# Kernel tuning notes

Measured on AMD Instinct MI355X. Metric: run time of the kernel, lower is better.

## Reference

```python
import jax, jax.numpy as jnp
import numpy as np

N = 100000   # nodes
DEG = 16     # in-degree per node
E = N * DEG  # edges
D = 64       # embedding_dim


def mobius_addition(x, y, c):
    xy = jnp.sum(x * y, axis=-1, keepdims=True)
    x2 = jnp.sum(x * x, axis=-1, keepdims=True)
    y2 = jnp.sum(y * y, axis=-1, keepdims=True)
    num = (1 + 2 * c * xy + c * y2) * x + (1 - c * x2) * y
    den = 1 + 2 * c * xy + c * c * x2 * y2
    return num / den


def exp_map(x, v, c):
    vn = jnp.linalg.norm(v, axis=-1, keepdims=True)
    sc = jnp.sqrt(c)
    second = jnp.tanh(sc * vn / 2) * v / (sc * vn)
    return mobius_addition(x, second, c)


def log_map(x, y, c):
    add = mobius_addition(-x, y, c)
    an = jnp.linalg.norm(add, axis=-1, keepdims=True)
    sc = jnp.sqrt(c)
    return 2 / sc * jnp.arctanh(sc * an) * add / an


def setup_inputs() -> dict:
    key = jax.random.key(0)
    ks = jax.random.split(key, 6)
    # scale so points are well inside the Poincare ball (atanh domain)
    x = jax.random.normal(ks[0], (N, D), jnp.float32) * 0.01
    src = jax.random.randint(ks[1], (E,), 0, N, dtype=jnp.int32)
    # every node gets exactly DEG in-edges -> no isolated nodes (avoids 0/0 in exp_map)
    dst = jnp.repeat(jnp.arange(N, dtype=jnp.int32), DEG)
    s = 1.0 / np.sqrt(D)
    Wq = jax.random.normal(ks[2], (D, D), jnp.float32) * s
    Wk = jax.random.normal(ks[3], (D, D), jnp.float32) * s
    Wv = jax.random.normal(ks[4], (D, D), jnp.float32) * s
    bq = jnp.zeros((D,), jnp.float32)
    bk = jnp.zeros((D,), jnp.float32)
    bv = jnp.zeros((D,), jnp.float32)
    curvature = jnp.ones((1,), jnp.float32)
    return {"x": x, "curvature": curvature, "Wq": Wq, "bq": bq, "Wk": Wk,
            "bk": bk, "Wv": Wv, "bv": bv, "src": src, "dst": dst}


def reference(x, curvature, Wq, bq, Wk, bk, Wv, bv, src, dst):
    c = curvature  # (1,), broadcasts against (N,1) keepdim norms
    n = x.shape[0]
    origin = jnp.zeros_like(x[:1])  # (1, D)
    tangent = log_map(origin, x, c)  # (N, D)
    # torch nn.Linear: y = x @ W.T + b
    q = tangent @ Wq.T + bq
    k = tangent @ Wk.T + bk
    v = tangent @ Wv.T + bv
    scale = jnp.asarray(x.shape[-1] ** 0.5, x.dtype)
    # per-edge score: <k[src], q[dst]> / sqrt(d)
    scores = jnp.einsum('ed,ed->e', k[src], q[dst]) / scale  # (E,)
    # segment (per-dst) softmax over incoming edges
    smax = jax.ops.segment_max(scores, dst, num_segments=n)
    ex = jnp.exp(scores - smax[dst])
    ssum = jax.ops.segment_sum(ex, dst, num_segments=n)
    alpha = ex / ssum[dst]  # (E,)
    # weighted scatter-sum of src values
    h = jax.ops.segment_sum(alpha[:, None] * v[src], dst, num_segments=n)  # (N, D)
    return exp_map(origin, h, c)
```

## Files before the change

kernel.cpp:

```cpp
#include <hip/hip_runtime.h>
#include <hip/hip_bf16.h>
#include <math.h>


typedef __attribute__((ext_vector_type(8))) short bf16x8;
typedef __attribute__((ext_vector_type(4))) float f32x4;
typedef __attribute__((ext_vector_type(2))) float f32x2;

static __device__ __forceinline__ short f2bf(float f) {
    union { __hip_bfloat16 h; short s; } u; u.h = __float2bfloat16(f); return u.s;
}

#define UBCVT(F, SRC, IDX) asm("v_cvt_f32_ubyte" IDX " %0, %1" : "=v"(F) : "v"(SRC))

#define TSTRIDE 72
#define SQF     68
#define SKSTR   72
#define SVSTR   68

__global__ __launch_bounds__(256) void qkv_kernel(
    const float* __restrict__ x,
    const float* __restrict__ cur,
    const float* __restrict__ Wq, const float* __restrict__ bq,
    const float* __restrict__ Wk, const float* __restrict__ bk,
    const float* __restrict__ Wv, const float* __restrict__ bv,
    float* __restrict__ qf, unsigned char* __restrict__ kvl,
    float* __restrict__ vs, int N)
{
    __shared__ short tL[128 * TSTRIDE];
    __shared__ float sqf[16 * SQF];
    __shared__ unsigned char sk[16 * SKSTR];
    __shared__ float svf[16 * SVSTR];
    const int tid = threadIdx.x;
    const int w = tid >> 6, lane = tid & 63;
    const int blockBase = blockIdx.x * 128;
    const float sc = __builtin_amdgcn_sqrtf(cur[0]);

    const int rr = lane >> 2, p = lane & 3;
    #pragma unroll
    for (int it = 0; it < 2; ++it) {
        const int rloc = w * 32 + it * 16 + rr;
        int row = blockBase + rloc; if (row >= N) row = N - 1;
        const float4* xr = (const float4*)(x + (size_t)row * 64 + p * 16);
        float4 x0 = xr[0], x1 = xr[1], x2 = xr[2], x3 = xr[3];
        float pn = x0.x*x0.x + x0.y*x0.y + x0.z*x0.z + x0.w*x0.w
                 + x1.x*x1.x + x1.y*x1.y + x1.z*x1.z + x1.w*x1.w
                 + x2.x*x2.x + x2.y*x2.y + x2.z*x2.z + x2.w*x2.w
                 + x3.x*x3.x + x3.y*x3.y + x3.z*x3.z + x3.w*x3.w;
        pn += __shfl_xor(pn, 1, 64);
        pn += __shfl_xor(pn, 2, 64);
        float z = sc * __builtin_amdgcn_sqrtf(pn);
        float ts = (z > 1e-12f)
            ? (__logf((1.0f + z) * __builtin_amdgcn_rcpf(1.0f - z))
               * __builtin_amdgcn_rcpf(z))
            : 2.0f;
        bf16x8 t0, t1;
        t0[0]=f2bf(ts*x0.x); t0[1]=f2bf(ts*x0.y); t0[2]=f2bf(ts*x0.z); t0[3]=f2bf(ts*x0.w);
        t0[4]=f2bf(ts*x1.x); t0[5]=f2bf(ts*x1.y); t0[6]=f2bf(ts*x1.z); t0[7]=f2bf(ts*x1.w);
        t1[0]=f2bf(ts*x2.x); t1[1]=f2bf(ts*x2.y); t1[2]=f2bf(ts*x2.z); t1[3]=f2bf(ts*x2.w);
        t1[4]=f2bf(ts*x3.x); t1[5]=f2bf(ts*x3.y); t1[6]=f2bf(ts*x3.z); t1[7]=f2bf(ts*x3.w);
        bf16x8* dst = (bf16x8*)&tL[rloc * TSTRIDE + p * 16];
        dst[0] = t0; dst[1] = t1;
    }
    __syncthreads();

    const int n16 = lane & 15, quad = lane >> 4;
    bf16x8 Bf[3][2];
    float bias[3];
    int matv[3], col0v[3];
    #pragma unroll
    for (int tt = 0; tt < 3; ++tt) {
        const int tile = w * 3 + tt;
        const int mat = tile >> 2;
        const int col0 = (tile & 3) * 16;
        matv[tt] = mat; col0v[tt] = col0;
        const float* Wm = (mat == 0) ? Wq : (mat == 1) ? Wk : Wv;
        const float* bm = (mat == 0) ? bq : (mat == 1) ? bk : bv;
        const float* srcp = Wm + (col0 + n16) * 64 + quad * 8;
        #pragma unroll
        for (int h = 0; h < 2; ++h) {
            float4 a = *(const float4*)(srcp + h * 32);
            float4 b = *(const float4*)(srcp + h * 32 + 4);
            bf16x8 f;
            f[0]=f2bf(a.x); f[1]=f2bf(a.y); f[2]=f2bf(a.z); f[3]=f2bf(a.w);
            f[4]=f2bf(b.x); f[5]=f2bf(b.y); f[6]=f2bf(b.z); f[7]=f2bf(b.w);
            Bf[tt][h] = f;
        }
        bias[tt] = bm[col0 + n16];
    }

    const int crow = tid >> 4;
    const int c8   = tid & 15;

    for (int nt = 0; nt < 8; ++nt) {
        const short* ar = &tL[(nt * 16 + n16) * TSTRIDE + quad * 8];
        bf16x8 A0 = *(const bf16x8*)ar;
        bf16x8 A1 = *(const bf16x8*)(ar + 32);
        #pragma unroll
        for (int tt = 0; tt < 3; ++tt) {
            f32x4 acc = { bias[tt], bias[tt], bias[tt], bias[tt] };
            acc = __builtin_amdgcn_mfma_f32_16x16x32_bf16(A0, Bf[tt][0], acc, 0, 0, 0);
            acc = __builtin_amdgcn_mfma_f32_16x16x32_bf16(A1, Bf[tt][1], acc, 0, 0, 0);
            const int mat = matv[tt], col0 = col0v[tt];
            #pragma unroll
            for (int r4 = 0; r4 < 4; ++r4) {
                const int rl = quad * 4 + r4;
                const int c  = col0 + n16;
                if (mat == 0) {
                    sqf[rl * SQF + c] = acc[r4];
                } else if (mat == 1) {
                    int pk = __builtin_amdgcn_cvt_pk_fp8_f32(acc[r4], acc[r4], 0, false);
                    sk[rl * SKSTR + c] = (unsigned char)(pk & 0xff);
                } else {
                    svf[rl * SVSTR + c] = acc[r4];
                }
            }
        }
        __syncthreads();

        const int node = blockBase + nt * 16 + crow;
        {
            f32x4 v4 = *(const f32x4*)&svf[crow * SVSTR + c8 * 4];
            float m = fmaxf(fmaxf(fabsf(v4[0]), fabsf(v4[1])),
                            fmaxf(fabsf(v4[2]), fabsf(v4[3])));
            m = fmaxf(m, __shfl_xor(m, 1, 64));
            m = fmaxf(m, __shfl_xor(m, 2, 64));
            m = fmaxf(m, __shfl_xor(m, 4, 64));
            m = fmaxf(m, __shfl_xor(m, 8, 64));
            float rm = fmaxf(m, 1e-20f);
            float inv = 127.0f * __builtin_amdgcn_rcpf(rm);
            float scale = rm * (1.0f / 127.0f);
            int i0 = __float2int_rn(v4[0] * inv) + 128;
            int i1 = __float2int_rn(v4[1] * inv) + 128;
            int i2 = __float2int_rn(v4[2] * inv) + 128;
            int i3 = __float2int_rn(v4[3] * inv) + 128;
            unsigned pk = (unsigned)(i0 & 255) | ((unsigned)(i1 & 255) << 8)
                        | ((unsigned)(i2 & 255) << 16) | ((unsigned)(i3 & 255) << 24);
            if (node < N) {
                *(f32x4*)(qf + (size_t)node * 64 + c8 * 4) =
                    *(const f32x4*)&sqf[crow * SQF + c8 * 4];
                *(unsigned*)(kvl + (size_t)node * 128 + c8 * 4) =
                    *(const unsigned*)&sk[crow * SKSTR + c8 * 4];
                *(unsigned*)(kvl + (size_t)node * 128 + 64 + c8 * 4) = pk;
                if (c8 == 0) vs[node] = scale;
            }
        }
        __syncthreads();
    }
}

__global__ __launch_bounds__(256) void attn_kernel(
    const float* __restrict__ qf, const unsigned char* __restrict__ kvl,
    const float* __restrict__ vs, const int* __restrict__ src,
    const float* __restrict__ cur,
    float* __restrict__ out, int N)
{
    __shared__ float aA[4][2][16];
    const int tid = threadIdx.x;
    const int w = tid >> 6, lane = tid & 63;
    int n0 = blockIdx.x * 8 + w;
    int n1 = n0 + 4;
    if (n0 >= N) n0 = N - 1;
    if (n1 >= N) n1 = N - 1;

    const int j = lane >> 2, p = lane & 3;
    const int g = lane >> 4, m = lane & 15;
    const float c0 = cur[0];

    const int* srow0 = src + n0 * 16;
    const int* srow1 = src + n1 * 16;
    const int  sj0 = srow0[j];
    const int4 s40 = *(const int4*)(srow0 + (g << 2));
    const int  sj1 = srow1[j];
    const int4 s41 = *(const int4*)(srow1 + (g << 2));

    const unsigned dimoff = (unsigned)(m << 2);
    const unsigned v00 = ((unsigned)s40.x << 7) + dimoff;
    const unsigned v01 = ((unsigned)s40.y << 7) + dimoff;
    const unsigned v02 = ((unsigned)s40.z << 7) + dimoff;
    const unsigned v03 = ((unsigned)s40.w << 7) + dimoff;
    const unsigned vr00 = *(const unsigned*)(kvl + 64 + v00);
    const unsigned vr01 = *(const unsigned*)(kvl + 64 + v01);
    const unsigned vr02 = *(const unsigned*)(kvl + 64 + v02);
    const unsigned vr03 = *(const unsigned*)(kvl + 64 + v03);
    const unsigned v10 = ((unsigned)s41.x << 7) + dimoff;
    const unsigned v11 = ((unsigned)s41.y << 7) + dimoff;
    const unsigned v12 = ((unsigned)s41.z << 7) + dimoff;
    const unsigned v13 = ((unsigned)s41.w << 7) + dimoff;
    const unsigned vr10 = *(const unsigned*)(kvl + 64 + v10);
    const unsigned vr11 = *(const unsigned*)(kvl + 64 + v11);
    const unsigned vr12 = *(const unsigned*)(kvl + 64 + v12);
    const unsigned vr13 = *(const unsigned*)(kvl + 64 + v13);

    const unsigned ko0 = ((unsigned)sj0 << 7) + (unsigned)(p << 4);
    const unsigned ko1 = ((unsigned)sj1 << 7) + (unsigned)(p << 4);
    const uint4 kd0 = *(const uint4*)(kvl + ko0);
    const uint4 kd1 = *(const uint4*)(kvl + ko1);
    const float sjs0 = vs[sj0];
    const float sjs1 = vs[sj1];

    const float* qp0 = qf + (size_t)n0 * 64 + (p << 4);
    const float4 q00 = *(const float4*)(qp0);
    const float4 q01 = *(const float4*)(qp0 + 4);
    const float4 q02 = *(const float4*)(qp0 + 8);
    const float4 q03 = *(const float4*)(qp0 + 12);

    float acc0 = 0.f;
    {
        f32x2 k0 = __builtin_amdgcn_cvt_pk_f32_fp8(kd0.x, false);
        f32x2 k1 = __builtin_amdgcn_cvt_pk_f32_fp8(kd0.x, true);
        acc0 = fmaf(k0[0], q00.x, acc0); acc0 = fmaf(k0[1], q00.y, acc0);
        acc0 = fmaf(k1[0], q00.z, acc0); acc0 = fmaf(k1[1], q00.w, acc0);
        k0 = __builtin_amdgcn_cvt_pk_f32_fp8(kd0.y, false);
        k1 = __builtin_amdgcn_cvt_pk_f32_fp8(kd0.y, true);
        acc0 = fmaf(k0[0], q01.x, acc0); acc0 = fmaf(k0[1], q01.y, acc0);
        acc0 = fmaf(k1[0], q01.z, acc0); acc0 = fmaf(k1[1], q01.w, acc0);
        k0 = __builtin_amdgcn_cvt_pk_f32_fp8(kd0.z, false);
        k1 = __builtin_amdgcn_cvt_pk_f32_fp8(kd0.z, true);
        acc0 = fmaf(k0[0], q02.x, acc0); acc0 = fmaf(k0[1], q02.y, acc0);
        acc0 = fmaf(k1[0], q02.z, acc0); acc0 = fmaf(k1[1], q02.w, acc0);
        k0 = __builtin_amdgcn_cvt_pk_f32_fp8(kd0.w, false);
        k1 = __builtin_amdgcn_cvt_pk_f32_fp8(kd0.w, true);
        acc0 = fmaf(k0[0], q03.x, acc0); acc0 = fmaf(k0[1], q03.y, acc0);
        acc0 = fmaf(k1[0], q03.z, acc0); acc0 = fmaf(k1[1], q03.w, acc0);
    }

    const float* qp1 = qf + (size_t)n1 * 64 + (p << 4);
    const float4 q10 = *(const float4*)(qp1);
    const float4 q11 = *(const float4*)(qp1 + 4);
    const float4 q12 = *(const float4*)(qp1 + 8);
    const float4 q13 = *(const float4*)(qp1 + 12);

    acc0 += __shfl_xor(acc0, 1, 64);
    acc0 += __shfl_xor(acc0, 2, 64);
    float ex0 = __builtin_amdgcn_exp2f(acc0 * (0.125f * 1.44269504f));
    float ss0 = ex0;
    #pragma unroll
    for (int mm = 4; mm < 64; mm <<= 1) ss0 += __shfl_xor(ss0, mm, 64);
    float as0 = ex0 * sjs0 * __builtin_amdgcn_rcpf(ss0);
    if (p == 0) aA[w][0][j] = as0;

    float acc1 = 0.f;
    {
        f32x2 k0 = __builtin_amdgcn_cvt_pk_f32_fp8(kd1.x, false);
        f32x2 k1 = __builtin_amdgcn_cvt_pk_f32_fp8(kd1.x, true);
        acc1 = fmaf(k0[0], q10.x, acc1); acc1 = fmaf(k0[1], q10.y, acc1);
        acc1 = fmaf(k1[0], q10.z, acc1); acc1 = fmaf(k1[1], q10.w, acc1);
        k0 = __builtin_amdgcn_cvt_pk_f32_fp8(kd1.y, false);
        k1 = __builtin_amdgcn_cvt_pk_f32_fp8(kd1.y, true);
        acc1 = fmaf(k0[0], q11.x, acc1); acc1 = fmaf(k0[1], q11.y, acc1);
        acc1 = fmaf(k1[0], q11.z, acc1); acc1 = fmaf(k1[1], q11.w, acc1);
        k0 = __builtin_amdgcn_cvt_pk_f32_fp8(kd1.z, false);
        k1 = __builtin_amdgcn_cvt_pk_f32_fp8(kd1.z, true);
        acc1 = fmaf(k0[0], q12.x, acc1); acc1 = fmaf(k0[1], q12.y, acc1);
        acc1 = fmaf(k1[0], q12.z, acc1); acc1 = fmaf(k1[1], q12.w, acc1);
        k0 = __builtin_amdgcn_cvt_pk_f32_fp8(kd1.w, false);
        k1 = __builtin_amdgcn_cvt_pk_f32_fp8(kd1.w, true);
        acc1 = fmaf(k0[0], q13.x, acc1); acc1 = fmaf(k0[1], q13.y, acc1);
        acc1 = fmaf(k1[0], q13.z, acc1); acc1 = fmaf(k1[1], q13.w, acc1);
    }

    acc1 += __shfl_xor(acc1, 1, 64);
    acc1 += __shfl_xor(acc1, 2, 64);
    float ex1 = __builtin_amdgcn_exp2f(acc1 * (0.125f * 1.44269504f));
    float ss1 = ex1;
    #pragma unroll
    for (int mm = 4; mm < 64; mm <<= 1) ss1 += __shfl_xor(ss1, mm, 64);
    float as1 = ex1 * sjs1 * __builtin_amdgcn_rcpf(ss1);
    if (p == 0) aA[w][1][j] = as1;

    __builtin_amdgcn_wave_barrier();
    const float4 a40 = *(const float4*)&aA[w][0][g << 2];
    const float4 a41 = *(const float4*)&aA[w][1][g << 2];
    const float sa0 = (a40.x + a40.y) + (a40.z + a40.w);
    const float sa1 = (a41.x + a41.y) + (a41.z + a41.w);

    float h00 = 0.f, h01 = 0.f, h02 = 0.f, h03 = 0.f;
    float h10 = 0.f, h11 = 0.f, h12 = 0.f, h13 = 0.f;
    {
        float f0, f1, f2, f3;
        UBCVT(f0, vr00, "0"); UBCVT(f1, vr00, "1"); UBCVT(f2, vr00, "2"); UBCVT(f3, vr00, "3");
        h00 = fmaf(a40.x, f0, h00); h01 = fmaf(a40.x, f1, h01);
        h02 = fmaf(a40.x, f2, h02); h03 = fmaf(a40.x, f3, h03);
        UBCVT(f0, vr01, "0"); UBCVT(f1, vr01, "1"); UBCVT(f2, vr01, "2"); UBCVT(f3, vr01, "3");
        h00 = fmaf(a40.y, f0, h00); h01 = fmaf(a40.y, f1, h01);
        h02 = fmaf(a40.y, f2, h02); h03 = fmaf(a40.y, f3, h03);
        UBCVT(f0, vr02, "0"); UBCVT(f1, vr02, "1"); UBCVT(f2, vr02, "2"); UBCVT(f3, vr02, "3");
        h00 = fmaf(a40.z, f0, h00); h01 = fmaf(a40.z, f1, h01);
        h02 = fmaf(a40.z, f2, h02); h03 = fmaf(a40.z, f3, h03);
        UBCVT(f0, vr03, "0"); UBCVT(f1, vr03, "1"); UBCVT(f2, vr03, "2"); UBCVT(f3, vr03, "3");
        h00 = fmaf(a40.w, f0, h00); h01 = fmaf(a40.w, f1, h01);
        h02 = fmaf(a40.w, f2, h02); h03 = fmaf(a40.w, f3, h03);

        UBCVT(f0, vr10, "0"); UBCVT(f1, vr10, "1"); UBCVT(f2, vr10, "2"); UBCVT(f3, vr10, "3");
        h10 = fmaf(a41.x, f0, h10); h11 = fmaf(a41.x, f1, h11);
        h12 = fmaf(a41.x, f2, h12); h13 = fmaf(a41.x, f3, h13);
        UBCVT(f0, vr11, "0"); UBCVT(f1, vr11, "1"); UBCVT(f2, vr11, "2"); UBCVT(f3, vr11, "3");
        h10 = fmaf(a41.y, f0, h10); h11 = fmaf(a41.y, f1, h11);
        h12 = fmaf(a41.y, f2, h12); h13 = fmaf(a41.y, f3, h13);
        UBCVT(f0, vr12, "0"); UBCVT(f1, vr12, "1"); UBCVT(f2, vr12, "2"); UBCVT(f3, vr12, "3");
        h10 = fmaf(a41.z, f0, h10); h11 = fmaf(a41.z, f1, h11);
        h12 = fmaf(a41.z, f2, h12); h13 = fmaf(a41.z, f3, h13);
        UBCVT(f0, vr13, "0"); UBCVT(f1, vr13, "1"); UBCVT(f2, vr13, "2"); UBCVT(f3, vr13, "3");
        h10 = fmaf(a41.w, f0, h10); h11 = fmaf(a41.w, f1, h11);
        h12 = fmaf(a41.w, f2, h12); h13 = fmaf(a41.w, f3, h13);
    }
    const float cr0 = 128.0f * sa0;
    const float cr1 = 128.0f * sa1;
    h00 -= cr0; h01 -= cr0; h02 -= cr0; h03 -= cr0;
    h10 -= cr1; h11 -= cr1; h12 -= cr1; h13 -= cr1;

    h00 += __shfl_xor(h00, 16, 64); h01 += __shfl_xor(h01, 16, 64);
    h02 += __shfl_xor(h02, 16, 64); h03 += __shfl_xor(h03, 16, 64);
    h10 += __shfl_xor(h10, 16, 64); h11 += __shfl_xor(h11, 16, 64);
    h12 += __shfl_xor(h12, 16, 64); h13 += __shfl_xor(h13, 16, 64);
    h00 += __shfl_xor(h00, 32, 64); h01 += __shfl_xor(h01, 32, 64);
    h02 += __shfl_xor(h02, 32, 64); h03 += __shfl_xor(h03, 32, 64);
    h10 += __shfl_xor(h10, 32, 64); h11 += __shfl_xor(h11, 32, 64);
    h12 += __shfl_xor(h12, 32, 64); h13 += __shfl_xor(h13, 32, 64);

    float n20 = h00*h00 + h01*h01 + h02*h02 + h03*h03;
    float n21 = h10*h10 + h11*h11 + h12*h12 + h13*h13;
    n20 += __shfl_xor(n20, 1, 64); n21 += __shfl_xor(n21, 1, 64);
    n20 += __shfl_xor(n20, 2, 64); n21 += __shfl_xor(n21, 2, 64);
    n20 += __shfl_xor(n20, 4, 64); n21 += __shfl_xor(n21, 4, 64);
    n20 += __shfl_xor(n20, 8, 64); n21 += __shfl_xor(n21, 8, 64);
    const float sc = __builtin_amdgcn_sqrtf(c0);
    float z0 = sc * __builtin_amdgcn_sqrtf(n20);
    float z1 = sc * __builtin_amdgcn_sqrtf(n21);
    float e0 = __builtin_amdgcn_exp2f(z0 * 1.44269504f);
    float e1 = __builtin_amdgcn_exp2f(z1 * 1.44269504f);
    float sc0 = (z0 > 1e-12f)
        ? ((e0 - 1.0f) * __builtin_amdgcn_rcpf(z0 * (e0 + 1.0f))) : 0.5f;
    float sc1 = (z1 > 1e-12f)
        ? ((e1 - 1.0f) * __builtin_amdgcn_rcpf(z1 * (e1 + 1.0f))) : 0.5f;
    if (lane < 16) {
        float4 o0 = make_float4(sc0 * h00, sc0 * h01, sc0 * h02, sc0 * h03);
        float4 o1 = make_float4(sc1 * h10, sc1 * h11, sc1 * h12, sc1 * h13);
        *(float4*)(out + (size_t)n0 * 64 + (lane << 2)) = o0;
        *(float4*)(out + (size_t)n1 * 64 + (lane << 2)) = o1;
    }
}

extern "C" void kernel_launch(void* const* d_in, const int* in_sizes, int n_in,
                              void* d_out, int out_size, void* d_ws, size_t ws_size,
                              hipStream_t stream)
{
    const float* x   = (const float*)d_in[0];
    const float* cur = (const float*)d_in[1];
    const float* Wq  = (const float*)d_in[2];
    const float* bq  = (const float*)d_in[3];
    const float* Wk  = (const float*)d_in[4];
    const float* bk  = (const float*)d_in[5];
    const float* Wv  = (const float*)d_in[6];
    const float* bv  = (const float*)d_in[7];
    const int* src = (const int*)d_in[8];

    const int N = in_sizes[0] / 64;

    float*          qf  = (float*)d_ws;
    unsigned char*  kvl = (unsigned char*)(qf + (size_t)N * 64);
    float*          vsc = (float*)(kvl + (size_t)N * 128);

    const int blocks1 = (N + 127) / 128;
    const int blocks2 = (N + 7) / 8;
    qkv_kernel<<<blocks1, 256, 0, stream>>>(x, cur, Wq, bq, Wk, bk, Wv, bv,
                                            qf, kvl, vsc, N);
    attn_kernel<<<blocks2, 256, 0, stream>>>(qf, kvl, vsc, src, cur,
                                             (float*)d_out, N);
}
```

Measured before the change: 156.0 us.

## Store Q in bf16 and make attention kernel persistent with src prefetch

Q is now written by the projection kernel as bf16 instead of fp32, which halves Q write and read traffic, and the attention kernel widens it back to float with shifts. The attention kernel becomes a grid-stride persistent loop over a capped grid of 2048 blocks, with each wave handling two adjacent nodes and prefetching the next iteration's src indices. This cuts launch and tail overhead and overlaps index loads with compute, but it adds bf16 rounding error on Q and a loop-carried dependency that may limit latency hiding.

Measured after the change: 154.5 us. Within noise of the previous version (-0.9%).

```diff
diff --git a/kernel.cpp b/kernel.cpp
--- a/kernel.cpp
+++ b/kernel.cpp
@@ -10,11 +10,17 @@
 static __device__ __forceinline__ short f2bf(float f) {
     union { __hip_bfloat16 h; short s; } u; u.h = __float2bfloat16(f); return u.s;
 }
+static __device__ __forceinline__ float bflo(unsigned u) {
+    return __uint_as_float(u << 16);
+}
+static __device__ __forceinline__ float bfhi(unsigned u) {
+    return __uint_as_float(u & 0xffff0000u);
+}
 
 #define UBCVT(F, SRC, IDX) asm("v_cvt_f32_ubyte" IDX " %0, %1" : "=v"(F) : "v"(SRC))
 
 #define TSTRIDE 72
-#define SQF     68
+#define SQSTR   72
 #define SKSTR   72
 #define SVSTR   68
 
@@ -24,11 +30,11 @@
     const float* __restrict__ Wq, const float* __restrict__ bq,
     const float* __restrict__ Wk, const float* __restrict__ bk,
     const float* __restrict__ Wv, const float* __restrict__ bv,
-    float* __restrict__ qf, unsigned char* __restrict__ kvl,
+    unsigned short* __restrict__ qb, unsigned char* __restrict__ kvl,
     float* __restrict__ vs, int N)
 {
     __shared__ short tL[128 * TSTRIDE];
-    __shared__ float sqf[16 * SQF];
+    __shared__ short sq[16 * SQSTR];
     __shared__ unsigned char sk[16 * SKSTR];
     __shared__ float svf[16 * SVSTR];
     const int tid = threadIdx.x;
@@ -107,7 +113,7 @@
                 const int rl = quad * 4 + r4;
                 const int c  = col0 + n16;
                 if (mat == 0) {
-                    sqf[rl * SQF + c] = acc[r4];
+                    sq[rl * SQSTR + c] = f2bf(acc[r4]);
                 } else if (mat == 1) {
                     int pk = __builtin_amdgcn_cvt_pk_fp8_f32(acc[r4], acc[r4], 0, false);
                     sk[rl * SKSTR + c] = (unsigned char)(pk & 0xff);
@@ -137,8 +143,8 @@
             unsigned pk = (unsigned)(i0 & 255) | ((unsigned)(i1 & 255) << 8)
                         | ((unsigned)(i2 & 255) << 16) | ((unsigned)(i3 & 255) << 24);
             if (node < N) {
-                *(f32x4*)(qf + (size_t)node * 64 + c8 * 4) =
-                    *(const f32x4*)&sqf[crow * SQF + c8 * 4];
+                *(uint2*)(qb + (size_t)node * 64 + c8 * 4) =
+                    *(const uint2*)&sq[crow * SQSTR + c8 * 4];
                 *(unsigned*)(kvl + (size_t)node * 128 + c8 * 4) =
                     *(const unsigned*)&sk[crow * SKSTR + c8 * 4];
                 *(unsigned*)(kvl + (size_t)node * 128 + 64 + c8 * 4) = pk;
@@ -150,7 +156,7 @@
 }
 
 __global__ __launch_bounds__(256) void attn_kernel(
-    const float* __restrict__ qf, const unsigned char* __restrict__ kvl,
+    const unsigned short* __restrict__ qb, const unsigned char* __restrict__ kvl,
     const float* __restrict__ vs, const int* __restrict__ src,
     const float* __restrict__ cur,
     float* __restrict__ out, int N)
@@ -158,187 +164,198 @@
     __shared__ float aA[4][2][16];
     const int tid = threadIdx.x;
     const int w = tid >> 6, lane = tid & 63;
-    int n0 = blockIdx.x * 8 + w;
-    int n1 = n0 + 4;
-    if (n0 >= N) n0 = N - 1;
-    if (n1 >= N) n1 = N - 1;
+    const int wg = blockIdx.x * 4 + w;
+    const int stride = gridDim.x * 8;
 
     const int j = lane >> 2, p = lane & 3;
     const int g = lane >> 4, m = lane & 15;
     const float c0 = cur[0];
-
-    const int* srow0 = src + n0 * 16;
-    const int* srow1 = src + n1 * 16;
-    const int  sj0 = srow0[j];
-    const int4 s40 = *(const int4*)(srow0 + (g << 2));
-    const int  sj1 = srow1[j];
-    const int4 s41 = *(const int4*)(srow1 + (g << 2));
-
+    const float sc = __builtin_amdgcn_sqrtf(c0);
     const unsigned dimoff = (unsigned)(m << 2);
-    const unsigned v00 = ((unsigned)s40.x << 7) + dimoff;
-    const unsigned v01 = ((unsigned)s40.y << 7) + dimoff;
-    const unsigned v02 = ((unsigned)s40.z << 7) + dimoff;
-    const unsigned v03 = ((unsigned)s40.w << 7) + dimoff;
-    const unsigned vr00 = *(const unsigned*)(kvl + 64 + v00);
-    const unsigned vr01 = *(const unsigned*)(kvl + 64 + v01);
-    const unsigned vr02 = *(const unsigned*)(kvl + 64 + v02);
-    const unsigned vr03 = *(const unsigned*)(kvl + 64 + v03);
-    const unsigned v10 = ((unsigned)s41.x << 7) + dimoff;
-    const unsigned v11 = ((unsigned)s41.y << 7) + dimoff;
-    const unsigned v12 = ((unsigned)s41.z << 7) + dimoff;
-    const unsigned v13 = ((unsigned)s41.w << 7) + dimoff;
-    const unsigned vr10 = *(const unsigned*)(kvl + 64 + v10);
-    const unsigned vr11 = *(const unsigned*)(kvl + 64 + v11);
-    const unsigned vr12 = *(const unsigned*)(kvl + 64 + v12);
-    const unsigned vr13 = *(const unsigned*)(kvl + 64 + v13);
-
-    const unsigned ko0 = ((unsigned)sj0 << 7) + (unsigned)(p << 4);
-    const unsigned ko1 = ((unsigned)sj1 << 7) + (unsigned)(p << 4);
-    const uint4 kd0 = *(const uint4*)(kvl + ko0);
-    const uint4 kd1 = *(const uint4*)(kvl + ko1);
-    const float sjs0 = vs[sj0];
-    const float sjs1 = vs[sj1];
-
-    const float* qp0 = qf + (size_t)n0 * 64 + (p << 4);
-    const float4 q00 = *(const float4*)(qp0);
-    const float4 q01 = *(const float4*)(qp0 + 4);
-    const float4 q02 = *(const float4*)(qp0 + 8);
-    const float4 q03 = *(const float4*)(qp0 + 12);
-
-    float acc0 = 0.f;
-    {
-        f32x2 k0 = __builtin_amdgcn_cvt_pk_f32_fp8(kd0.x, false);
-        f32x2 k1 = __builtin_amdgcn_cvt_pk_f32_fp8(kd0.x, true);
-        acc0 = fmaf(k0[0], q00.x, acc0); acc0 = fmaf(k0[1], q00.y, acc0);
-        acc0 = fmaf(k1[0], q00.z, acc0); acc0 = fmaf(k1[1], q00.w, acc0);
-        k0 = __builtin_amdgcn_cvt_pk_f32_fp8(kd0.y, false);
-        k1 = __builtin_amdgcn_cvt_pk_f32_fp8(kd0.y, true);
-        acc0 = fmaf(k0[0], q01.x, acc0); acc0 = fmaf(k0[1], q01.y, acc0);
-        acc0 = fmaf(k1[0], q01.z, acc0); acc0 = fmaf(k1[1], q01.w, acc0);
-        k0 = __builtin_amdgcn_cvt_pk_f32_fp8(kd0.z, false);
-        k1 = __builtin_amdgcn_cvt_pk_f32_fp8(kd0.z, true);
-        acc0 = fmaf(k0[0], q02.x, acc0); acc0 = fmaf(k0[1], q02.y, acc0);
-        acc0 = fmaf(k1[0], q02.z, acc0); acc0 = fmaf(k1[1], q02.w, acc0);
-        k0 = __builtin_amdgcn_cvt_pk_f32_fp8(kd0.w, false);
-        k1 = __builtin_amdgcn_cvt_pk_f32_fp8(kd0.w, true);
-        acc0 = fmaf(k0[0], q03.x, acc0); acc0 = fmaf(k0[1], q03.y, acc0);
-        acc0 = fmaf(k1[0], q03.z, acc0); acc0 = fmaf(k1[1], q03.w, acc0);
-    }
-
-    const float* qp1 = qf + (size_t)n1 * 64 + (p << 4);
-    const float4 q10 = *(const float4*)(qp1);
-    const float4 q11 = *(const float4*)(qp1 + 4);
-    const float4 q12 = *(const float4*)(qp1 + 8);
-    const float4 q13 = *(const float4*)(qp1 + 12);
-
-    acc0 += __shfl_xor(acc0, 1, 64);
-    acc0 += __shfl_xor(acc0, 2, 64);
-    float ex0 = __builtin_amdgcn_exp2f(acc0 * (0.125f * 1.44269504f));
-    float ss0 = ex0;
-    #pragma unroll
-    for (int mm = 4; mm < 64; mm <<= 1) ss0 += __shfl_xor(ss0, mm, 64);
-    float as0 = ex0 * sjs0 * __builtin_amdgcn_rcpf(ss0);
-    if (p == 0) aA[w][0][j] = as0;
-
-    float acc1 = 0.f;
-    {
-        f32x2 k0 = __builtin_amdgcn_cvt_pk_f32_fp8(kd1.x, false);
-        f32x2 k1 = __builtin_amdgcn_cvt_pk_f32_fp8(kd1.x, true);
-        acc1 = fmaf(k0[0], q10.x, acc1); acc1 = fmaf(k0[1], q10.y, acc1);
-        acc1 = fmaf(k1[0], q10.z, acc1); acc1 = fmaf(k1[1], q10.w, acc1);
-        k0 = __builtin_amdgcn_cvt_pk_f32_fp8(kd1.y, false);
-        k1 = __builtin_amdgcn_cvt_pk_f32_fp8(kd1.y, true);
-        acc1 = fmaf(k0[0], q11.x, acc1); acc1 = fmaf(k0[1], q11.y, acc1);
-        acc1 = fmaf(k1[0], q11.z, acc1); acc1 = fmaf(k1[1], q11.w, acc1);
-        k0 = __builtin_amdgcn_cvt_pk_f32_fp8(kd1.z, false);
-        k1 = __builtin_amdgcn_cvt_pk_f32_fp8(kd1.z, true);
-        acc1 = fmaf(k0[0], q12.x, acc1); acc1 = fmaf(k0[1], q12.y, acc1);
-        acc1 = fmaf(k1[0], q12.z, acc1); acc1 = fmaf(k1[1], q12.w, acc1);
-        k0 = __builtin_amdgcn_cvt_pk_f32_fp8(kd1.w, false);
-        k1 = __builtin_amdgcn_cvt_pk_f32_fp8(kd1.w, true);
-        acc1 = fmaf(k0[0], q13.x, acc1); acc1 = fmaf(k0[1], q13.y, acc1);
-        acc1 = fmaf(k1[0], q13.z, acc1); acc1 = fmaf(k1[1], q13.w, acc1);
-    }
-
-    acc1 += __shfl_xor(acc1, 1, 64);
-    acc1 += __shfl_xor(acc1, 2, 64);
-    float ex1 = __builtin_amdgcn_exp2f(acc1 * (0.125f * 1.44269504f));
-    float ss1 = ex1;
-    #pragma unroll
-    for (int mm = 4; mm < 64; mm <<= 1) ss1 += __shfl_xor(ss1, mm, 64);
-    float as1 = ex1 * sjs1 * __builtin_amdgcn_rcpf(ss1);
-    if (p == 0) aA[w][1][j] = as1;
-
-    __builtin_amdgcn_wave_barrier();
-    const float4 a40 = *(const float4*)&aA[w][0][g << 2];
-    const float4 a41 = *(const float4*)&aA[w][1][g << 2];
-    const float sa0 = (a40.x + a40.y) + (a40.z + a40.w);
-    const float sa1 = (a41.x + a41.y) + (a41.z + a41.w);
-
-    float h00 = 0.f, h01 = 0.f, h02 = 0.f, h03 = 0.f;
-    float h10 = 0.f, h11 = 0.f, h12 = 0.f, h13 = 0.f;
-    {
-        float f0, f1, f2, f3;
-        UBCVT(f0, vr00, "0"); UBCVT(f1, vr00, "1"); UBCVT(f2, vr00, "2"); UBCVT(f3, vr00, "3");
-        h00 = fmaf(a40.x, f0, h00); h01 = fmaf(a40.x, f1, h01);
-        h02 = fmaf(a40.x, f2, h02); h03 = fmaf(a40.x, f3, h03);
-        UBCVT(f0, vr01, "0"); UBCVT(f1, vr01, "1"); UBCVT(f2, vr01, "2"); UBCVT(f3, vr01, "3");
-        h00 = fmaf(a40.y, f0, h00); h01 = fmaf(a40.y, f1, h01);
-        h02 = fmaf(a40.y, f2, h02); h03 = fmaf(a40.y, f3, h03);
-        UBCVT(f0, vr02, "0"); UBCVT(f1, vr02, "1"); UBCVT(f2, vr02, "2"); UBCVT(f3, vr02, "3");
-        h00 = fmaf(a40.z, f0, h00); h01 = fmaf(a40.z, f1, h01);
-        h02 = fmaf(a40.z, f2, h02); h03 = fmaf(a40.z, f3, h03);
-        UBCVT(f0, vr03, "0"); UBCVT(f1, vr03, "1"); UBCVT(f2, vr03, "2"); UBCVT(f3, vr03, "3");
-        h00 = fmaf(a40.w, f0, h00); h01 = fmaf(a40.w, f1, h01);
-        h02 = fmaf(a40.w, f2, h02); h03 = fmaf(a40.w, f3, h03);
-
-        UBCVT(f0, vr10, "0"); UBCVT(f1, vr10, "1"); UBCVT(f2, vr10, "2"); UBCVT(f3, vr10, "3");
-        h10 = fmaf(a41.x, f0, h10); h11 = fmaf(a41.x, f1, h11);
-        h12 = fmaf(a41.x, f2, h12); h13 = fmaf(a41.x, f3, h13);
-        UBCVT(f0, vr11, "0"); UBCVT(f1, vr11, "1"); UBCVT(f2, vr11, "2"); UBCVT(f3, vr11, "3");
-        h10 = fmaf(a41.y, f0, h10); h11 = fmaf(a41.y, f1, h11);
-        h12 = fmaf(a41.y, f2, h12); h13 = fmaf(a41.y, f3, h13);
-        UBCVT(f0, vr12, "0"); UBCVT(f1, vr12, "1"); UBCVT(f2, vr12, "2"); UBCVT(f3, vr12, "3");
-        h10 = fmaf(a41.z, f0, h10); h11 = fmaf(a41.z, f1, h11);
-        h12 = fmaf(a41.z, f2, h12); h13 = fmaf(a41.z, f3, h13);
-        UBCVT(f0, vr13, "0"); UBCVT(f1, vr13, "1"); UBCVT(f2, vr13, "2"); UBCVT(f3, vr13, "3");
-        h10 = fmaf(a41.w, f0, h10); h11 = fmaf(a41.w, f1, h11);
-        h12 = fmaf(a41.w, f2, h12); h13 = fmaf(a41.w, f3, h13);
-    }
-    const float cr0 = 128.0f * sa0;
-    const float cr1 = 128.0f * sa1;
-    h00 -= cr0; h01 -= cr0; h02 -= cr0; h03 -= cr0;
-    h10 -= cr1; h11 -= cr1; h12 -= cr1; h13 -= cr1;
-
-    h00 += __shfl_xor(h00, 16, 64); h01 += __shfl_xor(h01, 16, 64);
-    h02 += __shfl_xor(h02, 16, 64); h03 += __shfl_xor(h03, 16, 64);
-    h10 += __shfl_xor(h10, 16, 64); h11 += __shfl_xor(h11, 16, 64);
-    h12 += __shfl_xor(h12, 16, 64); h13 += __shfl_xor(h13, 16, 64);
-    h00 += __shfl_xor(h00, 32, 64); h01 += __shfl_xor(h01, 32, 64);
-    h02 += __shfl_xor(h02, 32, 64); h03 += __shfl_xor(h03, 32, 64);
-    h10 += __shfl_xor(h10, 32, 64); h11 += __shfl_xor(h11, 32, 64);
-    h12 += __shfl_xor(h12, 32, 64); h13 += __shfl_xor(h13, 32, 64);
-
-    float n20 = h00*h00 + h01*h01 + h02*h02 + h03*h03;
-    float n21 = h10*h10 + h11*h11 + h12*h12 + h13*h13;
-    n20 += __shfl_xor(n20, 1, 64); n21 += __shfl_xor(n21, 1, 64);
-    n20 += __shfl_xor(n20, 2, 64); n21 += __shfl_xor(n21, 2, 64);
-    n20 += __shfl_xor(n20, 4, 64); n21 += __shfl_xor(n21, 4, 64);
-    n20 += __shfl_xor(n20, 8, 64); n21 += __shfl_xor(n21, 8, 64);
-    const float sc = __builtin_amdgcn_sqrtf(c0);
-    float z0 = sc * __builtin_amdgcn_sqrtf(n20);
-    float z1 = sc * __builtin_amdgcn_sqrtf(n21);
-    float e0 = __builtin_amdgcn_exp2f(z0 * 1.44269504f);
-    float e1 = __builtin_amdgcn_exp2f(z1 * 1.44269504f);
-    float sc0 = (z0 > 1e-12f)
-        ? ((e0 - 1.0f) * __builtin_amdgcn_rcpf(z0 * (e0 + 1.0f))) : 0.5f;
-    float sc1 = (z1 > 1e-12f)
-        ? ((e1 - 1.0f) * __builtin_amdgcn_rcpf(z1 * (e1 + 1.0f))) : 0.5f;
-    if (lane < 16) {
-        float4 o0 = make_float4(sc0 * h00, sc0 * h01, sc0 * h02, sc0 * h03);
-        float4 o1 = make_float4(sc1 * h10, sc1 * h11, sc1 * h12, sc1 * h13);
-        *(float4*)(out + (size_t)n0 * 64 + (lane << 2)) = o0;
-        *(float4*)(out + (size_t)n1 * 64 + (lane << 2)) = o1;
+
+    int n0 = wg * 2;
+    if (n0 >= N) return;
+
+    int  sjA0 = src[n0 * 16 + j];
+    int  sjA1 = src[n0 * 16 + 16 + j];
+    int4 s4A0 = *(const int4*)(src + n0 * 16 + (g << 2));
+    int4 s4A1 = *(const int4*)(src + n0 * 16 + 16 + (g << 2));
+
+    while (true) {
+        const int n1 = n0 + 1;
+        const int nn = n0 + stride;
+        const int sj0 = sjA0, sj1 = sjA1;
+        const int4 s40 = s4A0, s41 = s4A1;
+
+        const unsigned vo00 = ((unsigned)s40.x << 7) + dimoff;
+        const unsigned vo01 = ((unsigned)s40.y << 7) + dimoff;
+        const unsigned vo02 = ((unsigned)s40.z << 7) + dimoff;
+        const unsigned vo03 = ((unsigned)s40.w << 7) + dimoff;
+        const unsigned vr00 = *(const unsigned*)(kvl + 64 + vo00);
+        const unsigned vr01 = *(const unsigned*)(kvl + 64 + vo01);
+        const unsigned vr02 = *(const unsigned*)(kvl + 64 + vo02);
+        const unsigned vr03 = *(const unsigned*)(kvl + 64 + vo03);
+        const unsigned vo10 = ((unsigned)s41.x << 7) + dimoff;
+        const unsigned vo11 = ((unsigned)s41.y << 7) + dimoff;
+        const unsigned vo12 = ((unsigned)s41.z << 7) + dimoff;
+        const unsigned vo13 = ((unsigned)s41.w << 7) + dimoff;
+        const unsigned vr10 = *(const unsigned*)(kvl + 64 + vo10);
+        const unsigned vr11 = *(const unsigned*)(kvl + 64 + vo11);
+        const unsigned vr12 = *(const unsigned*)(kvl + 64 + vo12);
+        const unsigned vr13 = *(const unsigned*)(kvl + 64 + vo13);
+
+        const unsigned ko0 = ((unsigned)sj0 << 7) + (unsigned)(p << 4);
+        const unsigned ko1 = ((unsigned)sj1 << 7) + (unsigned)(p << 4);
+        const uint4 kd0 = *(const uint4*)(kvl + ko0);
+        const uint4 kd1 = *(const uint4*)(kvl + ko1);
+        const float sjs0 = vs[sj0];
+        const float sjs1 = vs[sj1];
+
+        const uint4* qp0 = (const uint4*)(qb + (size_t)n0 * 64 + (p << 4));
+        const uint4 qa0 = qp0[0], qc0 = qp0[1];
+        const uint4* qp1 = (const uint4*)(qb + (size_t)n1 * 64 + (p << 4));
+        const uint4 qa1 = qp1[0], qc1 = qp1[1];
+
+        int sjB0, sjB1; int4 s4B0, s4B1;
+        const bool more = (nn < N);
+        if (more) {
+            sjB0 = src[nn * 16 + j];
+            sjB1 = src[nn * 16 + 16 + j];
+            s4B0 = *(const int4*)(src + nn * 16 + (g << 2));
+            s4B1 = *(const int4*)(src + nn * 16 + 16 + (g << 2));
+        }
+
+        float acc0 = 0.f;
+        {
+            f32x2 k0 = __builtin_amdgcn_cvt_pk_f32_fp8(kd0.x, false);
+            f32x2 k1 = __builtin_amdgcn_cvt_pk_f32_fp8(kd0.x, true);
+            acc0 = fmaf(k0[0], bflo(qa0.x), acc0); acc0 = fmaf(k0[1], bfhi(qa0.x), acc0);
+            acc0 = fmaf(k1[0], bflo(qa0.y), acc0); acc0 = fmaf(k1[1], bfhi(qa0.y), acc0);
+            k0 = __builtin_amdgcn_cvt_pk_f32_fp8(kd0.y, false);
+            k1 = __builtin_amdgcn_cvt_pk_f32_fp8(kd0.y, true);
+            acc0 = fmaf(k0[0], bflo(qa0.z), acc0); acc0 = fmaf(k0[1], bfhi(qa0.z), acc0);
+            acc0 = fmaf(k1[0], bflo(qa0.w), acc0); acc0 = fmaf(k1[1], bfhi(qa0.w), acc0);
+            k0 = __builtin_amdgcn_cvt_pk_f32_fp8(kd0.z, false);
+            k1 = __builtin_amdgcn_cvt_pk_f32_fp8(kd0.z, true);
+            acc0 = fmaf(k0[0], bflo(qc0.x), acc0); acc0 = fmaf(k0[1], bfhi(qc0.x), acc0);
+            acc0 = fmaf(k1[0], bflo(qc0.y), acc0); acc0 = fmaf(k1[1], bfhi(qc0.y), acc0);
+            k0 = __builtin_amdgcn_cvt_pk_f32_fp8(kd0.w, false);
+            k1 = __builtin_amdgcn_cvt_pk_f32_fp8(kd0.w, true);
+            acc0 = fmaf(k0[0], bflo(qc0.z), acc0); acc0 = fmaf(k0[1], bfhi(qc0.z), acc0);
+            acc0 = fmaf(k1[0], bflo(qc0.w), acc0); acc0 = fmaf(k1[1], bfhi(qc0.w), acc0);
+        }
+        acc0 += __shfl_xor(acc0, 1, 64);
+        acc0 += __shfl_xor(acc0, 2, 64);
+        float ex0 = __builtin_amdgcn_exp2f(acc0 * (0.125f * 1.44269504f));
+        float ss0 = ex0;
+        #pragma unroll
+        for (int mm = 4; mm < 64; mm <<= 1) ss0 += __shfl_xor(ss0, mm, 64);
+        float as0 = ex0 * sjs0 * __builtin_amdgcn_rcpf(ss0);
+        if (p == 0) aA[w][0][j] = as0;
+
+        float acc1 = 0.f;
+        {
+            f32x2 k0 = __builtin_amdgcn_cvt_pk_f32_fp8(kd1.x, false);
+            f32x2 k1 = __builtin_amdgcn_cvt_pk_f32_fp8(kd1.x, true);
+            acc1 = fmaf(k0[0], bflo(qa1.x), acc1); acc1 = fmaf(k0[1], bfhi(qa1.x), acc1);
+            acc1 = fmaf(k1[0], bflo(qa1.y), acc1); acc1 = fmaf(k1[1], bfhi(qa1.y), acc1);
+            k0 = __builtin_amdgcn_cvt_pk_f32_fp8(kd1.y, false);
+            k1 = __builtin_amdgcn_cvt_pk_f32_fp8(kd1.y, true);
+            acc1 = fmaf(k0[0], bflo(qa1.z), acc1); acc1 = fmaf(k0[1], bfhi(qa1.z), acc1);
+            acc1 = fmaf(k1[0], bflo(qa1.w), acc1); acc1 = fmaf(k1[1], bfhi(qa1.w), acc1);
+            k0 = __builtin_amdgcn_cvt_pk_f32_fp8(kd1.z, false);
+            k1 = __builtin_amdgcn_cvt_pk_f32_fp8(kd1.z, true);
+            acc1 = fmaf(k0[0], bflo(qc1.x), acc1); acc1 = fmaf(k0[1], bfhi(qc1.x), acc1);
+            acc1 = fmaf(k1[0], bflo(qc1.y), acc1); acc1 = fmaf(k1[1], bfhi(qc1.y), acc1);
+            k0 = __builtin_amdgcn_cvt_pk_f32_fp8(kd1.w, false);
+            k1 = __builtin_amdgcn_cvt_pk_f32_fp8(kd1.w, true);
+            acc1 = fmaf(k0[0], bflo(qc1.z), acc1); acc1 = fmaf(k0[1], bfhi(qc1.z), acc1);
+            acc1 = fmaf(k1[0], bflo(qc1.w), acc1); acc1 = fmaf(k1[1], bfhi(qc1.w), acc1);
+        }
+        acc1 += __shfl_xor(acc1, 1, 64);
+        acc1 += __shfl_xor(acc1, 2, 64);
+        float ex1 = __builtin_amdgcn_exp2f(acc1 * (0.125f * 1.44269504f));
+        float ss1 = ex1;
+        #pragma unroll
+        for (int mm = 4; mm < 64; mm <<= 1) ss1 += __shfl_xor(ss1, mm, 64);
+        float as1 = ex1 * sjs1 * __builtin_amdgcn_rcpf(ss1);
+        if (p == 0) aA[w][1][j] = as1;
+
+        __builtin_amdgcn_wave_barrier();
+        const float4 a40 = *(const float4*)&aA[w][0][g << 2];
+        const float4 a41 = *(const float4*)&aA[w][1][g << 2];
+        __builtin_amdgcn_wave_barrier();
+        const float sa0 = (a40.x + a40.y) + (a40.z + a40.w);
+        const float sa1 = (a41.x + a41.y) + (a41.z + a41.w);
+
+        float h00 = 0.f, h01 = 0.f, h02 = 0.f, h03 = 0.f;
+        float h10 = 0.f, h11 = 0.f, h12 = 0.f, h13 = 0.f;
+        {
+            float f0, f1, f2, f3;
+            UBCVT(f0, vr00, "0"); UBCVT(f1, vr00, "1"); UBCVT(f2, vr00, "2"); UBCVT(f3, vr00, "3");
+            h00 = fmaf(a40.x, f0, h00); h01 = fmaf(a40.x, f1, h01);
+            h02 = fmaf(a40.x, f2, h02); h03 = fmaf(a40.x, f3, h03);
+            UBCVT(f0, vr01, "0"); UBCVT(f1, vr01, "1"); UBCVT(f2, vr01, "2"); UBCVT(f3, vr01, "3");
+            h00 = fmaf(a40.y, f0, h00); h01 = fmaf(a40.y, f1, h01);
+            h02 = fmaf(a40.y, f2, h02); h03 = fmaf(a40.y, f3, h03);
+            UBCVT(f0, vr02, "0"); UBCVT(f1, vr02, "1"); UBCVT(f2, vr02, "2"); UBCVT(f3, vr02, "3");
+            h00 = fmaf(a40.z, f0, h00); h01 = fmaf(a40.z, f1, h01);
+            h02 = fmaf(a40.z, f2, h02); h03 = fmaf(a40.z, f3, h03);
+            UBCVT(f0, vr03, "0"); UBCVT(f1, vr03, "1"); UBCVT(f2, vr03, "2"); UBCVT(f3, vr03, "3");
+            h00 = fmaf(a40.w, f0, h00); h01 = fmaf(a40.w, f1, h01);
+            h02 = fmaf(a40.w, f2, h02); h03 = fmaf(a40.w, f3, h03);
+
+            UBCVT(f0, vr10, "0"); UBCVT(f1, vr10, "1"); UBCVT(f2, vr10, "2"); UBCVT(f3, vr10, "3");
+            h10 = fmaf(a41.x, f0, h10); h11 = fmaf(a41.x, f1, h11);
+            h12 = fmaf(a41.x, f2, h12); h13 = fmaf(a41.x, f3, h13);
+            UBCVT(f0, vr11, "0"); UBCVT(f1, vr11, "1"); UBCVT(f2, vr11, "2"); UBCVT(f3, vr11, "3");
+            h10 = fmaf(a41.y, f0, h10); h11 = fmaf(a41.y, f1, h11);
+            h12 = fmaf(a41.y, f2, h12); h13 = fmaf(a41.y, f3, h13);
+            UBCVT(f0, vr12, "0"); UBCVT(f1, vr12, "1"); UBCVT(f2, vr12, "2"); UBCVT(f3, vr12, "3");
+            h10 = fmaf(a41.z, f0, h10); h11 = fmaf(a41.z, f1, h11);
+            h12 = fmaf(a41.z, f2, h12); h13 = fmaf(a41.z, f3, h13);
+            UBCVT(f0, vr13, "0"); UBCVT(f1, vr13, "1"); UBCVT(f2, vr13, "2"); UBCVT(f3, vr13, "3");
+            h10 = fmaf(a41.w, f0, h10); h11 = fmaf(a41.w, f1, h11);
+            h12 = fmaf(a41.w, f2, h12); h13 = fmaf(a41.w, f3, h13);
+        }
+        const float cr0 = 128.0f * sa0;
+        const float cr1 = 128.0f * sa1;
+        h00 -= cr0; h01 -= cr0; h02 -= cr0; h03 -= cr0;
+        h10 -= cr1; h11 -= cr1; h12 -= cr1; h13 -= cr1;
+
+        h00 += __shfl_xor(h00, 16, 64); h01 += __shfl_xor(h01, 16, 64);
+        h02 += __shfl_xor(h02, 16, 64); h03 += __shfl_xor(h03, 16, 64);
+        h10 += __shfl_xor(h10, 16, 64); h11 += __shfl_xor(h11, 16, 64);
+        h12 += __shfl_xor(h12, 16, 64); h13 += __shfl_xor(h13, 16, 64);
+        h00 += __shfl_xor(h00, 32, 64); h01 += __shfl_xor(h01, 32, 64);
+        h02 += __shfl_xor(h02, 32, 64); h03 += __shfl_xor(h03, 32, 64);
+        h10 += __shfl_xor(h10, 32, 64); h11 += __shfl_xor(h11, 32, 64);
+        h12 += __shfl_xor(h12, 32, 64); h13 += __shfl_xor(h13, 32, 64);
+
+        float n20 = h00*h00 + h01*h01 + h02*h02 + h03*h03;
+        float n21 = h10*h10 + h11*h11 + h12*h12 + h13*h13;
+        n20 += __shfl_xor(n20, 1, 64); n21 += __shfl_xor(n21, 1, 64);
+        n20 += __shfl_xor(n20, 2, 64); n21 += __shfl_xor(n21, 2, 64);
+        n20 += __shfl_xor(n20, 4, 64); n21 += __shfl_xor(n21, 4, 64);
+        n20 += __shfl_xor(n20, 8, 64); n21 += __shfl_xor(n21, 8, 64);
+        float z0 = sc * __builtin_amdgcn_sqrtf(n20);
+        float z1 = sc * __builtin_amdgcn_sqrtf(n21);
+        float e0 = __builtin_amdgcn_exp2f(z0 * 1.44269504f);
+        float e1 = __builtin_amdgcn_exp2f(z1 * 1.44269504f);
+        float sc0 = (z0 > 1e-12f)
+            ? ((e0 - 1.0f) * __builtin_amdgcn_rcpf(z0 * (e0 + 1.0f))) : 0.5f;
+        float sc1 = (z1 > 1e-12f)
+            ? ((e1 - 1.0f) * __builtin_amdgcn_rcpf(z1 * (e1 + 1.0f))) : 0.5f;
+        if (lane < 16) {
+            float4 o0 = make_float4(sc0 * h00, sc0 * h01, sc0 * h02, sc0 * h03);
+            float4 o1 = make_float4(sc1 * h10, sc1 * h11, sc1 * h12, sc1 * h13);
+            *(float4*)(out + (size_t)n0 * 64 + (lane << 2)) = o0;
+            *(float4*)(out + (size_t)n1 * 64 + (lane << 2)) = o1;
+        }
+
+        if (!more) break;
+        n0 = nn;
+        sjA0 = sjB0; sjA1 = sjB1; s4A0 = s4B0; s4A1 = s4B1;
     }
 }
 
@@ -358,14 +375,16 @@
 
     const int N = in_sizes[0] / 64;
 
-    float*          qf  = (float*)d_ws;
-    unsigned char*  kvl = (unsigned char*)(qf + (size_t)N * 64);
+    unsigned short* qb  = (unsigned short*)d_ws;
+    unsigned char*  kvl = (unsigned char*)(qb + (size_t)N * 64);
     float*          vsc = (float*)(kvl + (size_t)N * 128);
 
     const int blocks1 = (N + 127) / 128;
-    const int blocks2 = (N + 7) / 8;
+    int blocks2 = 2048;
+    const int need = (N + 7) / 8;
+    if (blocks2 > need) blocks2 = need;
     qkv_kernel<<<blocks1, 256, 0, stream>>>(x, cur, Wq, bq, Wk, bk, Wv, bv,
-                                            qf, kvl, vsc, N);
-    attn_kernel<<<blocks2, 256, 0, stream>>>(qf, kvl, vsc, src, cur,
+                                            qb, kvl, vsc, N);
+    attn_kernel<<<blocks2, 256, 0, stream>>>(qb, kvl, vsc, src, cur,
                                              (float*)d_out, N);
 }
```
